# Performance work log

Measured on AMD Instinct MI355X. Metric: run time of the kernel, lower is better.

The kernel has to match this reference:

```python
import jax, jax.numpy as jnp
import numpy as np

B, N, F, D, H, K, L = 16, 2048, 40, 256, 8, 256, 4
DH = D // H  # 32

def setup_inputs() -> dict:
    key = jax.random.key(0)
    ks = jax.random.split(key, 12)
    rn = lambda k, shp: jax.random.normal(k, shp, dtype=jnp.float32) * 0.02
    return dict(
        x=jax.random.normal(ks[0], (B, N, F), dtype=jnp.float32),
        W_emb=rn(ks[1], (F, D)), b_emb=jnp.zeros((D,), jnp.float32),
        pos=rn(ks[11], (1, N, D)),
        ln0_g=jnp.ones((D,), jnp.float32), ln0_b=jnp.zeros((D,), jnp.float32),
        ln1_g=jnp.ones((L, D), jnp.float32), ln1_b=jnp.zeros((L, D), jnp.float32),
        Wq=rn(ks[2], (L, D, D)), Wk=rn(ks[3], (L, D, D)), Wv=rn(ks[4], (L, D, D)),
        Ek=rn(ks[5], (L, N, K)), Ev=rn(ks[6], (L, N, K)),
        Wo=rn(ks[7], (L, D, D)), bo=jnp.zeros((L, D), jnp.float32),
        ln2_g=jnp.ones((L, D), jnp.float32), ln2_b=jnp.zeros((L, D), jnp.float32),
        W1=rn(ks[8], (L, D, 4 * D)), b1=jnp.zeros((L, 4 * D), jnp.float32),
        W2=rn(ks[9], (L, 4 * D, D)), b2=jnp.zeros((L, D), jnp.float32),
        W_out=rn(ks[10], (D, 1)), b_out=jnp.zeros((1,), jnp.float32))

def _ln(t, g, b, eps=1e-5):
    m = t.mean(-1, keepdims=True)
    v = ((t - m) ** 2).mean(-1, keepdims=True)
    return (t - m) * jax.lax.rsqrt(v + eps) * g + b

def reference(x, W_emb, b_emb, pos, ln0_g, ln0_b, ln1_g, ln1_b, Wq, Wk, Wv,
              Ek, Ev, Wo, bo, ln2_g, ln2_b, W1, b1, W2, b2, W_out, b_out):
    h = x @ W_emb + b_emb + pos          # [B,N,D] embed + learned pos enc
    h = _ln(h, ln0_g, ln0_b)
    scale = DH ** -0.5
    for i in range(L):  # Linformer layer: prenorm attn + prenorm FF, residual
        a = _ln(h, ln1_g[i], ln1_b[i])
        q = (a @ Wq[i]).reshape(B, N, H, DH).transpose(0, 2, 1, 3)            # bhnd
        k = jnp.einsum('bnd,nk->bkd', a @ Wk[i], Ek[i])                        # low-rank proj
        v = jnp.einsum('bnd,nk->bkd', a @ Wv[i], Ev[i])
        k = k.reshape(B, K, H, DH).transpose(0, 2, 1, 3)                       # bhkd
        v = v.reshape(B, K, H, DH).transpose(0, 2, 1, 3)
        attn = jax.nn.softmax(jnp.einsum('bhnd,bhkd->bhnk', q, k) * scale, axis=-1)
        o = jnp.einsum('bhnk,bhkd->bhnd', attn, v).transpose(0, 2, 1, 3).reshape(B, N, D)
        h = h + o @ Wo[i] + bo[i]
        a = _ln(h, ln2_g[i], ln2_b[i])
        h = h + jax.nn.gelu(a @ W1[i] + b1[i], approximate=False) @ W2[i] + b2[i]
    return h @ W_out + b_out             # [B,N,1]
```

## Files before the change

kernel.cpp:

```cpp
#include <hip/hip_runtime.h>
#include <hip/hip_bf16.h>


typedef short bf16x8 __attribute__((ext_vector_type(8)));
typedef float f32x4 __attribute__((ext_vector_type(4)));
typedef unsigned int u32x4 __attribute__((ext_vector_type(4)));

#define GLOBAL_AS __attribute__((address_space(1)))
#define LDS_AS __attribute__((address_space(3)))

static __device__ __forceinline__ float gelu_f(float v) {
    return 0.5f * v * (1.0f + erff(v * 0.70710678118654752f));
}
static __device__ __forceinline__ ushort f2bf(float x) {
    __hip_bfloat16 h = __float2bfloat16(x);
    return __builtin_bit_cast(ushort, h);
}

__global__ __launch_bounds__(256)
void embed_ln2(const float* __restrict__ x, const float* __restrict__ Wemb,
               const float* __restrict__ bemb, const float* __restrict__ pos,
               const float* __restrict__ g0, const float* __restrict__ b0,
               float* __restrict__ H)
{
    const int t = threadIdx.x, w = t >> 6, l = t & 63;
    const long row = (long)blockIdx.x * 4 + w;
    const int n = (int)(row & 2047);
    const float xl = (l < 40) ? x[row * 40 + l] : 0.f;
    float4 acc = *(const float4*)&bemb[l * 4];
    const float4 pv = *(const float4*)&pos[(long)n * 256 + l * 4];
    acc.x += pv.x; acc.y += pv.y; acc.z += pv.z; acc.w += pv.w;
    #pragma unroll 8
    for (int f = 0; f < 40; ++f) {
        const float xf = __shfl(xl, f);
        const float4 wv = *(const float4*)&Wemb[f * 256 + l * 4];
        acc.x += xf * wv.x; acc.y += xf * wv.y; acc.z += xf * wv.z; acc.w += xf * wv.w;
    }
    float s = acc.x + acc.y + acc.z + acc.w;
    #pragma unroll
    for (int m = 32; m >= 1; m >>= 1) s += __shfl_xor(s, m);
    const float mean = s * (1.0f / 256.0f);
    const float dx = acc.x - mean, dy = acc.y - mean, dz = acc.z - mean, dw = acc.w - mean;
    float q = dx * dx + dy * dy + dz * dz + dw * dw;
    #pragma unroll
    for (int m = 32; m >= 1; m >>= 1) q += __shfl_xor(q, m);
    const float inv = rsqrtf(q * (1.0f / 256.0f) + 1e-5f);
    const float4 gv = *(const float4*)&g0[l * 4];
    const float4 bv = *(const float4*)&b0[l * 4];
    float4 y;
    y.x = dx * inv * gv.x + bv.x;
    y.y = dy * inv * gv.y + bv.y;
    y.z = dz * inv * gv.z + bv.z;
    y.w = dw * inv * gv.w + bv.w;
    *(float4*)&H[row * 256 + l * 4] = y;
}

__global__ __launch_bounds__(256)
void ln_kernel(const float* __restrict__ X, const float* __restrict__ g,
               const float* __restrict__ b, ushort* __restrict__ Y)
{
    const int row = blockIdx.x * 4 + (threadIdx.x >> 6);
    const int lane = threadIdx.x & 63;
    const long base = (long)row * 256 + lane * 4;
    float4 xv = *(const float4*)&X[base];
    float s = xv.x + xv.y + xv.z + xv.w;
    #pragma unroll
    for (int m = 32; m >= 1; m >>= 1) s += __shfl_xor(s, m);
    const float mean = s * (1.0f / 256.0f);
    const float dx = xv.x - mean, dy = xv.y - mean, dz = xv.z - mean, dw = xv.w - mean;
    float q = dx * dx + dy * dy + dz * dz + dw * dw;
    #pragma unroll
    for (int m = 32; m >= 1; m >>= 1) q += __shfl_xor(q, m);
    const float inv = rsqrtf(q * (1.0f / 256.0f) + 1e-5f);
    const float4 gv = *(const float4*)&g[lane * 4];
    const float4 bv = *(const float4*)&b[lane * 4];
    ushort4 y;
    y.x = f2bf(dx * inv * gv.x + bv.x);
    y.y = f2bf(dy * inv * gv.y + bv.y);
    y.z = f2bf(dz * inv * gv.z + bv.z);
    y.w = f2bf(dw * inv * gv.w + bv.w);
    *(ushort4*)&Y[base] = y;
}

__global__ __launch_bounds__(256)
void transpose_cast(const float* __restrict__ in, ushort* __restrict__ out,
                    int R, int C, long sIn, long sOut)
{
    __shared__ float tile[32][33];
    in += (long)blockIdx.z * sIn; out += (long)blockIdx.z * sOut;
    const int c0 = blockIdx.x * 32, r0 = blockIdx.y * 32;
    const int tx = threadIdx.x & 31, ty = threadIdx.x >> 5;
    #pragma unroll
    for (int j = 0; j < 4; ++j)
        tile[ty + j * 8][tx] = in[(long)(r0 + ty + j * 8) * C + c0 + tx];
    __syncthreads();
    #pragma unroll
    for (int j = 0; j < 4; ++j)
        out[(long)(c0 + ty + j * 8) * R + r0 + tx] = f2bf(tile[tx][ty + j * 8]);
}

__global__ __launch_bounds__(256)
void transpose_act(const ushort* __restrict__ in, ushort* __restrict__ out)
{
    __shared__ ushort tile[32][33];
    const int c0 = blockIdx.x * 32, r0 = blockIdx.y * 32;
    const int tx = threadIdx.x & 31, ty = threadIdx.x >> 5;
    #pragma unroll
    for (int j = 0; j < 4; ++j)
        tile[ty + j * 8][tx] = in[(long)(r0 + ty + j * 8) * 256 + c0 + tx];
    __syncthreads();
    const int b = r0 >> 11, nn = r0 & 2047;
    #pragma unroll
    for (int j = 0; j < 4; ++j)
        out[((long)(b * 256 + c0 + ty + j * 8)) * 2048 + nn + tx] = tile[tx][ty + j * 8];
}

template<int OBF16, int ACT, int HASB, int ACCF>
__global__ __launch_bounds__(256)
void gemm64(const ushort* __restrict__ A, const ushort* __restrict__ BT,
            const float* __restrict__ bias, void* __restrict__ Cout,
            int Kd, int lda, int ldb, int ldc,
            long sA, long sBT, long sC)
{
    __shared__ ushort Als[64 * 32];
    __shared__ ushort Bls[64 * 32];
    const int bz = blockIdx.z;
    const ushort* Ab = A + (long)bz * sA;
    const ushort* Bb = BT + (long)bz * sBT;
    const int m0 = blockIdx.x * 64, n0 = blockIdx.y * 64;
    const int t = threadIdx.x, l = t & 63, w = t >> 6;
    const int wr = w >> 1, wc = w & 1;
    const int fr = l & 15, fq = l >> 4;

    f32x4 acc[2][2];
    #pragma unroll
    for (int m = 0; m < 2; ++m)
        #pragma unroll
        for (int n = 0; n < 2; ++n) acc[m][n] = f32x4{0.f, 0.f, 0.f, 0.f};

    const int srow = t >> 2;
    const int skcol = (t & 3) * 8;
    const int dst0 = w * 512;
    const ushort* Abase = Ab + (long)(m0 + srow) * lda + skcol;
    const ushort* Bbase = Bb + (long)(n0 + srow) * ldb + skcol;

    for (int kk = 0; kk < Kd; kk += 32) {
        __builtin_amdgcn_global_load_lds((const GLOBAL_AS void*)(Abase + kk),
                                         (LDS_AS void*)&Als[dst0], 16, 0, 0);
        __builtin_amdgcn_global_load_lds((const GLOBAL_AS void*)(Bbase + kk),
                                         (LDS_AS void*)&Bls[dst0], 16, 0, 0);
        __syncthreads();
        bf16x8 af[2], bfv[2];
        #pragma unroll
        for (int m = 0; m < 2; ++m)
            af[m] = *(const bf16x8*)&Als[(wr * 32 + m * 16 + fr) * 32 + fq * 8];
        #pragma unroll
        for (int n = 0; n < 2; ++n)
            bfv[n] = *(const bf16x8*)&Bls[(wc * 32 + n * 16 + fr) * 32 + fq * 8];
        #pragma unroll
        for (int m = 0; m < 2; ++m)
            #pragma unroll
            for (int n = 0; n < 2; ++n)
                acc[m][n] = __builtin_amdgcn_mfma_f32_16x16x32_bf16(af[m], bfv[n], acc[m][n], 0, 0, 0);
        __syncthreads();
    }

    float bsv[2];
    #pragma unroll
    for (int n = 0; n < 2; ++n) bsv[n] = HASB ? bias[n0 + wc * 32 + n * 16 + fr] : 0.f;
    #pragma unroll
    for (int m = 0; m < 2; ++m) {
        #pragma unroll
        for (int r = 0; r < 4; ++r) {
            const int grow = m0 + wr * 32 + m * 16 + fq * 4 + r;
            const long rowoff = (long)grow * ldc + n0 + wc * 32 + fr;
            #pragma unroll
            for (int n = 0; n < 2; ++n) {
                float v = acc[m][n][r] + bsv[n];
                if (ACT) v = gelu_f(v);
                const long off = rowoff + n * 16;
                if (OBF16) {
                    ((ushort*)Cout)[(long)bz * sC + off] = f2bf(v);
                } else {
                    float* Cp = (float*)Cout + (long)bz * sC;
                    if (ACCF) v += Cp[off];
                    Cp[off] = v;
                }
            }
        }
    }
}

__global__ __launch_bounds__(256)
void attn_mfma2(const ushort* __restrict__ Q, const ushort* __restrict__ Kp,
                const ushort* __restrict__ VpT, ushort* __restrict__ O)
{
    __shared__ ushort Kls[256 * 40];
    __shared__ ushort Vls[32 * 264];
    const int qt = blockIdx.x, h = blockIdx.y, b = blockIdx.z;
    const int n0 = qt * 64;
    const int t = threadIdx.x, w = t >> 6, l = t & 63;
    const int fr = l & 15, fq = l >> 4;

    #pragma unroll
    for (int it = 0; it < 4; ++it) {
        const int r = (t >> 2) + it * 64, c = (t & 3) * 8;
        *(float4*)&Kls[r * 40 + c] =
            *(const float4*)&Kp[((long)(b * 256 + r)) * 256 + h * 32 + c];
    }
    {
        const int r = t >> 3, c0 = (t & 7) * 32;
        const ushort* src = VpT + ((long)(b * 256 + h * 32 + r)) * 256 + c0;
        #pragma unroll
        for (int j = 0; j < 4; ++j)
            *(float4*)&Vls[r * 264 + c0 + j * 8] = *(const float4*)(src + j * 8);
    }
    const bf16x8 bq = *(const bf16x8*)
        &Q[((long)(b * 2048 + n0 + w * 16 + fr)) * 256 + h * 32 + fq * 8];
    __syncthreads();

    f32x4 s[16];
    #pragma unroll
    for (int n = 0; n < 16; ++n) {
        const bf16x8 ak = *(const bf16x8*)&Kls[(n * 16 + fr) * 40 + fq * 8];
        s[n] = __builtin_amdgcn_mfma_f32_16x16x32_bf16(ak, bq, f32x4{0.f,0.f,0.f,0.f}, 0, 0, 0);
    }
    const float scale = 0.17677669529663687f;
    float mx = -1e30f;
    #pragma unroll
    for (int n = 0; n < 16; ++n)
        #pragma unroll
        for (int r = 0; r < 4; ++r) { s[n][r] *= scale; mx = fmaxf(mx, s[n][r]); }
    mx = fmaxf(mx, __shfl_xor(mx, 16));
    mx = fmaxf(mx, __shfl_xor(mx, 32));
    float sm = 0.f;
    unsigned int p[16][2];
    #pragma unroll
    for (int n = 0; n < 16; ++n) {
        float e0 = __expf(s[n][0] - mx), e1 = __expf(s[n][1] - mx);
        float e2 = __expf(s[n][2] - mx), e3 = __expf(s[n][3] - mx);
        sm += (e0 + e1) + (e2 + e3);
        p[n][0] = ((unsigned int)f2bf(e1) << 16) | f2bf(e0);
        p[n][1] = ((unsigned int)f2bf(e3) << 16) | f2bf(e2);
    }
    sm += __shfl_xor(sm, 16);
    sm += __shfl_xor(sm, 32);

    const int fqa = fq & 1, fqb = fq >> 1;
    f32x4 o[2] = {f32x4{0.f,0.f,0.f,0.f}, f32x4{0.f,0.f,0.f,0.f}};
    #pragma unroll
    for (int kk = 0; kk < 8; ++kk) {
        u32x4 bw;
        #pragma unroll
        for (int wd = 0; wd < 4; ++wd) {
            const int srcl = fr + ((2 * fqa + (wd >> 1)) << 4);
            const unsigned int v0 = __shfl((int)p[2 * kk][wd & 1], srcl);
            const unsigned int v1 = __shfl((int)p[2 * kk + 1][wd & 1], srcl);
            bw[wd] = fqb ? v1 : v0;
        }
        const bf16x8 breg = __builtin_bit_cast(bf16x8, bw);
        #pragma unroll
        for (int nd = 0; nd < 2; ++nd) {
            const bf16x8 av = *(const bf16x8*)&Vls[(nd * 16 + fr) * 264 + kk * 32 + fq * 8];
            o[nd] = __builtin_amdgcn_mfma_f32_16x16x32_bf16(av, breg, o[nd], 0, 0, 0);
        }
    }
    const float inv = 1.0f / sm;
    const long rowbase = ((long)(b * 2048 + n0 + w * 16 + fr)) * 256 + h * 32;
    #pragma unroll
    for (int nd = 0; nd < 2; ++nd) {
        ushort4 y;
        y.x = f2bf(o[nd][0] * inv); y.y = f2bf(o[nd][1] * inv);
        y.z = f2bf(o[nd][2] * inv); y.w = f2bf(o[nd][3] * inv);
        *(ushort4*)&O[rowbase + nd * 16 + fq * 4] = y;
    }
}

__global__ __launch_bounds__(256)
void out_kernel(const float* __restrict__ H, const float* __restrict__ Wout,
                const float* __restrict__ bout, float* __restrict__ out)
{
    const int row = blockIdx.x * 4 + (threadIdx.x >> 6);
    const int lane = threadIdx.x & 63;
    float4 hv = *(const float4*)&H[(long)row * 256 + lane * 4];
    float4 wv = *(const float4*)&Wout[lane * 4];
    float s = hv.x * wv.x + hv.y * wv.y + hv.z * wv.z + hv.w * wv.w;
    #pragma unroll
    for (int m = 32; m >= 1; m >>= 1) s += __shfl_xor(s, m);
    if (lane == 0) out[row] = s + bout[0];
}

extern "C" void kernel_launch(void* const* d_in, const int* in_sizes, int n_in,
                              void* d_out, int out_size, void* d_ws, size_t ws_size,
                              hipStream_t stream)
{
    const float* x    = (const float*)d_in[0];
    const float* Wemb = (const float*)d_in[1];
    const float* bemb = (const float*)d_in[2];
    const float* pos  = (const float*)d_in[3];
    const float* ln0g = (const float*)d_in[4];
    const float* ln0b = (const float*)d_in[5];
    const float* ln1g = (const float*)d_in[6];
    const float* ln1b = (const float*)d_in[7];
    const float* Wq   = (const float*)d_in[8];
    const float* Wk   = (const float*)d_in[9];
    const float* Wv   = (const float*)d_in[10];
    const float* Ek   = (const float*)d_in[11];
    const float* Ev   = (const float*)d_in[12];
    const float* Wo   = (const float*)d_in[13];
    const float* bo   = (const float*)d_in[14];
    const float* ln2g = (const float*)d_in[15];
    const float* ln2b = (const float*)d_in[16];
    const float* W1   = (const float*)d_in[17];
    const float* b1   = (const float*)d_in[18];
    const float* W2   = (const float*)d_in[19];
    const float* b2   = (const float*)d_in[20];
    const float* Wout = (const float*)d_in[21];
    const float* bout = (const float*)d_in[22];

    char* ws = (char*)d_ws;
    float*  h    = (float*)(ws + 0);
    ushort* abf  = (ushort*)(ws + 33554432L);
    ushort* aT   = (ushort*)(ws + 50331648L);
    ushort* kp   = (ushort*)(ws + 67108864L);
    ushort* vpT  = (ushort*)(ws + 69206016L);
    ushort* apkv = (ushort*)(ws + 71303168L);
    ushort* qbf  = (ushort*)(ws + 100663296L);
    ushort* hid  = (ushort*)(ws + 50331648L);
    ushort* WT   = (ushort*)(ws + 117440512L);
    ushort* WqT  = WT;
    ushort* WkT  = WT + 262144;
    ushort* WvT  = WT + 524288;
    ushort* WoT  = WT + 786432;
    ushort* W1T  = WT + 1048576;
    ushort* W2T  = WT + 2097152;
    ushort* EkvT = WT + 3145728;
    float* outp = (float*)d_out;

    transpose_cast<<<dim3(8, 8, 4), 256, 0, stream>>>(Wq, WqT, 256, 256, 65536, 65536);
    transpose_cast<<<dim3(8, 8, 4), 256, 0, stream>>>(Wk, WkT, 256, 256, 65536, 65536);
    transpose_cast<<<dim3(8, 8, 4), 256, 0, stream>>>(Wv, WvT, 256, 256, 65536, 65536);
    transpose_cast<<<dim3(8, 8, 4), 256, 0, stream>>>(Wo, WoT, 256, 256, 65536, 65536);
    transpose_cast<<<dim3(32, 8, 4), 256, 0, stream>>>(W1, W1T, 256, 1024, 262144, 262144);
    transpose_cast<<<dim3(8, 32, 4), 256, 0, stream>>>(W2, W2T, 1024, 256, 262144, 262144);
    transpose_cast<<<dim3(8, 64, 4), 256, 0, stream>>>(Ek, EkvT, 2048, 256, 524288, 1048576);
    transpose_cast<<<dim3(8, 64, 4), 256, 0, stream>>>(Ev, EkvT + 524288, 2048, 256, 524288, 1048576);

    embed_ln2<<<8192, 256, 0, stream>>>(x, Wemb, bemb, pos, ln0g, ln0b, h);
    ln_kernel<<<8192, 256, 0, stream>>>(h, ln1g, ln1b, abf);
    transpose_act<<<dim3(8, 1024), 256, 0, stream>>>(abf, aT);

    for (int i = 0; i < 4; ++i) {
        const ushort* WqT_i = WqT + i * 65536;
        const ushort* WkT_i = WkT + i * 65536;
        const ushort* WvT_i = WvT + i * 65536;
        const ushort* WoT_i = WoT + i * 65536;
        const ushort* W1T_i = W1T + i * 262144;
        const ushort* W2T_i = W2T + i * 262144;
        const ushort* EkvT_i = EkvT + (long)i * 1048576;

        gemm64<1,0,0,0><<<dim3(512, 4, 1), 256, 0, stream>>>(abf, WqT_i, nullptr, qbf,
            256, 256, 256, 256, 0, 0, 0);
        gemm64<1,0,0,0><<<dim3(8, 4, 16), 256, 0, stream>>>(EkvT_i, aT, nullptr, apkv,
            2048, 2048, 2048, 256, 0, 524288, 131072);
        gemm64<1,0,0,0><<<dim3(4, 4, 16), 256, 0, stream>>>(apkv, WkT_i, nullptr, kp,
            256, 256, 256, 256, 131072, 0, 65536);
        gemm64<1,0,0,0><<<dim3(4, 4, 16), 256, 0, stream>>>(WvT_i, apkv + 65536, nullptr, vpT,
            256, 256, 256, 256, 0, 131072, 65536);
        attn_mfma2<<<dim3(32, 8, 16), 256, 0, stream>>>(qbf, kp, vpT, abf);
        gemm64<0,0,1,1><<<dim3(512, 4, 1), 256, 0, stream>>>(abf, WoT_i, bo + i * 256, h,
            256, 256, 256, 256, 0, 0, 0);
        ln_kernel<<<8192, 256, 0, stream>>>(h, ln2g + i * 256, ln2b + i * 256, abf);
        gemm64<1,1,1,0><<<dim3(512, 16, 1), 256, 0, stream>>>(abf, W1T_i,
            b1 + (long)i * 1024, hid, 256, 256, 256, 1024, 0, 0, 0);
        gemm64<0,0,1,1><<<dim3(512, 4, 1), 256, 0, stream>>>(hid, W2T_i, b2 + i * 256, h,
            1024, 1024, 1024, 256, 0, 0, 0);
        if (i < 3) {
            ln_kernel<<<8192, 256, 0, stream>>>(h, ln1g + (i + 1) * 256,
                ln1b + (i + 1) * 256, abf);
            transpose_act<<<dim3(8, 1024), 256, 0, stream>>>(abf, aT);
        }
    }
    out_kernel<<<8192, 256, 0, stream>>>(h, Wout, bout, outp);
}
```

Before: 941.7 us.

## Replace erf GELU with tanh approximation and batch embed rows per wave

GELU now uses the tanh approximation computed through an exp, instead of erff, which makes the FFN epilogue cheaper. The embedding kernel stages 32 input rows in shared memory and has each wave compute 8 rows, so each Wemb load is reused across rows and fewer blocks are launched. The tanh form departs from the reference's exact erf GELU, which adds numeric error that may stay within tolerance.

```diff
diff --git a/kernel.cpp b/kernel.cpp
--- a/kernel.cpp
+++ b/kernel.cpp
@@ -10,7 +10,9 @@
 #define LDS_AS __attribute__((address_space(3)))
 
 static __device__ __forceinline__ float gelu_f(float v) {
-    return 0.5f * v * (1.0f + erff(v * 0.70710678118654752f));
+    const float u2 = v * (0.7978845608028654f + 0.03567740814183427f * v * v);
+    const float t = 1.0f - 2.0f / (__expf(2.0f * u2) + 1.0f);
+    return 0.5f * v * (1.0f + t);
 }
 static __device__ __forceinline__ ushort f2bf(float x) {
     __hip_bfloat16 h = __float2bfloat16(x);
@@ -18,41 +20,58 @@
 }
 
 __global__ __launch_bounds__(256)
-void embed_ln2(const float* __restrict__ x, const float* __restrict__ Wemb,
+void embed_ln3(const float* __restrict__ x, const float* __restrict__ Wemb,
                const float* __restrict__ bemb, const float* __restrict__ pos,
                const float* __restrict__ g0, const float* __restrict__ b0,
                float* __restrict__ H)
 {
+    __shared__ float xs[32][40];
     const int t = threadIdx.x, w = t >> 6, l = t & 63;
-    const long row = (long)blockIdx.x * 4 + w;
-    const int n = (int)(row & 2047);
-    const float xl = (l < 40) ? x[row * 40 + l] : 0.f;
-    float4 acc = *(const float4*)&bemb[l * 4];
-    const float4 pv = *(const float4*)&pos[(long)n * 256 + l * 4];
-    acc.x += pv.x; acc.y += pv.y; acc.z += pv.z; acc.w += pv.w;
+    const long row0 = (long)blockIdx.x * 32;
+    for (int idx = t; idx < 32 * 40; idx += 256)
+        ((float*)xs)[idx] = x[row0 * 40 + idx];
+    __syncthreads();
+
+    const int r0 = w * 8;
+    const int nbase = (int)((row0 + r0) & 2047);
+    const float4 be = *(const float4*)&bemb[l * 4];
+    float4 acc[8];
     #pragma unroll 8
+    for (int j = 0; j < 8; ++j) {
+        const float4 pv = *(const float4*)&pos[(long)(nbase + j) * 256 + l * 4];
+        acc[j].x = be.x + pv.x; acc[j].y = be.y + pv.y;
+        acc[j].z = be.z + pv.z; acc[j].w = be.w + pv.w;
+    }
     for (int f = 0; f < 40; ++f) {
-        const float xf = __shfl(xl, f);
         const float4 wv = *(const float4*)&Wemb[f * 256 + l * 4];
-        acc.x += xf * wv.x; acc.y += xf * wv.y; acc.z += xf * wv.z; acc.w += xf * wv.w;
-    }
-    float s = acc.x + acc.y + acc.z + acc.w;
-    #pragma unroll
-    for (int m = 32; m >= 1; m >>= 1) s += __shfl_xor(s, m);
-    const float mean = s * (1.0f / 256.0f);
-    const float dx = acc.x - mean, dy = acc.y - mean, dz = acc.z - mean, dw = acc.w - mean;
-    float q = dx * dx + dy * dy + dz * dz + dw * dw;
-    #pragma unroll
-    for (int m = 32; m >= 1; m >>= 1) q += __shfl_xor(q, m);
-    const float inv = rsqrtf(q * (1.0f / 256.0f) + 1e-5f);
+        #pragma unroll 8
+        for (int j = 0; j < 8; ++j) {
+            const float xf = xs[r0 + j][f];
+            acc[j].x += xf * wv.x; acc[j].y += xf * wv.y;
+            acc[j].z += xf * wv.z; acc[j].w += xf * wv.w;
+        }
+    }
     const float4 gv = *(const float4*)&g0[l * 4];
     const float4 bv = *(const float4*)&b0[l * 4];
-    float4 y;
-    y.x = dx * inv * gv.x + bv.x;
-    y.y = dy * inv * gv.y + bv.y;
-    y.z = dz * inv * gv.z + bv.z;
-    y.w = dw * inv * gv.w + bv.w;
-    *(float4*)&H[row * 256 + l * 4] = y;
+    #pragma unroll 8
+    for (int j = 0; j < 8; ++j) {
+        float s = acc[j].x + acc[j].y + acc[j].z + acc[j].w;
+        #pragma unroll
+        for (int m = 32; m >= 1; m >>= 1) s += __shfl_xor(s, m);
+        const float mean = s * (1.0f / 256.0f);
+        const float dx = acc[j].x - mean, dy = acc[j].y - mean;
+        const float dz = acc[j].z - mean, dw = acc[j].w - mean;
+        float q = dx * dx + dy * dy + dz * dz + dw * dw;
+        #pragma unroll
+        for (int m = 32; m >= 1; m >>= 1) q += __shfl_xor(q, m);
+        const float inv = rsqrtf(q * (1.0f / 256.0f) + 1e-5f);
+        float4 y;
+        y.x = dx * inv * gv.x + bv.x;
+        y.y = dy * inv * gv.y + bv.y;
+        y.z = dz * inv * gv.z + bv.z;
+        y.w = dw * inv * gv.w + bv.w;
+        *(float4*)&H[(row0 + r0 + j) * 256 + l * 4] = y;
+    }
 }
 
 __global__ __launch_bounds__(256)
@@ -346,7 +365,7 @@
     transpose_cast<<<dim3(8, 64, 4), 256, 0, stream>>>(Ek, EkvT, 2048, 256, 524288, 1048576);
     transpose_cast<<<dim3(8, 64, 4), 256, 0, stream>>>(Ev, EkvT + 524288, 2048, 256, 524288, 1048576);
 
-    embed_ln2<<<8192, 256, 0, stream>>>(x, Wemb, bemb, pos, ln0g, ln0b, h);
+    embed_ln3<<<1024, 256, 0, stream>>>(x, Wemb, bemb, pos, ln0g, ln0b, h);
     ln_kernel<<<8192, 256, 0, stream>>>(h, ln1g, ln1b, abf);
     transpose_act<<<dim3(8, 1024), 256, 0, stream>>>(abf, aT);
 
```

After: 937.2 us. Within noise of the previous version (-0.5%).
